# Kernel optimization log

Hardware: AMD Instinct MI355X
Metric: run time of the kernel (lower is better)

The kernel has to match this reference:

```python
import jax, jax.numpy as jnp
import numpy as np

K = 16
BN_EPS = 1e-3  # keras BatchNormalization default epsilon
LRELU_ALPHA = 0.1


def _lrelu(x):
    return jnp.where(x > 0, x, LRELU_ALPHA * x)


def _bn(x, gamma, beta):
    # training-mode batch norm over all axes except the last (channels)
    axes = tuple(range(x.ndim - 1))
    m = jnp.mean(x, axis=axes)
    v = jnp.var(x, axis=axes)
    return gamma * (x - m) * jax.lax.rsqrt(v + BN_EPS) + beta


def setup_inputs() -> dict:
    key = jax.random.key(0)
    ks = jax.random.split(key, 14)
    N, P, Cp, C0 = 32, 1024, 3, 64
    channels = [128, 128, 256]
    inp = {
        "points": jax.random.normal(ks[0], (N, P, Cp), dtype=jnp.float32),
        "features": jax.random.normal(ks[1], (N, P, C0), dtype=jnp.float32),
    }
    # edge-conv 1x1 weights (no bias, with_bn=True); glorot-ish scaling
    c_in = 2 * C0
    for i, c_out in enumerate(channels):
        scale = (2.0 / (c_in + c_out)) ** 0.5
        inp[f"W{i}"] = jax.random.normal(ks[2 + i], (c_in, c_out), dtype=jnp.float32) * scale
        inp[f"g{i}"] = jnp.ones((c_out,), dtype=jnp.float32)
        inp[f"b{i}"] = jnp.zeros((c_out,), dtype=jnp.float32)
        c_in = c_out
    # shortcut 1x1 conv C0 -> channels[-1]
    scale = (2.0 / (C0 + channels[-1])) ** 0.5
    inp["Wsc"] = jax.random.normal(ks[10], (C0, channels[-1]), dtype=jnp.float32) * scale
    inp["gsc"] = jnp.ones((channels[-1],), dtype=jnp.float32)
    inp["bsc"] = jnp.zeros((channels[-1],), dtype=jnp.float32)
    return inp


def reference(points, features, W0, g0, b0, W1, g1, b1, W2, g2, b2, Wsc, gsc, bsc):
    # pairwise squared distance matrix D: (N, P, P)
    r = jnp.sum(points * points, axis=-1)
    D = r[:, :, None] - 2.0 * jnp.einsum("npc,nqc->npq", points, points) + r[:, None, :]
    # kNN indices, excluding self (first neighbor)
    _, idx = jax.lax.top_k(-D, K + 1)
    idx = idx[:, :, 1:]  # (N, P, K)
    # gather neighbor features per batch element -> (N, P, K, C0)
    knn_fts = jax.vmap(lambda f, i: f[i])(features, idx)
    center = jnp.broadcast_to(features[:, :, None, :], knn_fts.shape)
    x = jnp.concatenate([center, knn_fts - center], axis=-1)  # (N, P, K, 2*C0)
    for W, g, b in ((W0, g0, b0), (W1, g1, b1), (W2, g2, b2)):
        x = _lrelu(_bn(jnp.einsum("npkc,cd->npkd", x, W), g, b))
    fts = jnp.mean(x, axis=2)  # average pooling over K -> (N, P, C_out)
    sc = _bn(jnp.einsum("npc,cd->npd", features, Wsc), gsc, bsc)
    return _lrelu(sc + fts)
```

## Files before the change

kernel.cpp:

```cpp
#include <hip/hip_runtime.h>
#include <stdint.h>

typedef __bf16 bf16x8 __attribute__((ext_vector_type(8)));
typedef float f32x4 __attribute__((ext_vector_type(4)));

union FragU { uint4 q; bf16x8 v; };

__device__ __forceinline__ float bf2f(uint32_t h){
  union U{uint32_t u; float f;} x; x.u = h<<16; return x.f;
}
__device__ __forceinline__ uint32_t f2bf(float f){
  union U{float f; uint32_t u;} x; x.f=f;
  return (x.u + 0x7FFFu + ((x.u>>16)&1u)) >> 16;
}
__device__ __forceinline__ float lrelu(float x){ return fmaxf(x, 0.1f*x); }

__global__ __launch_bounds__(256) void knn_kernel(const float* __restrict__ points, int* __restrict__ idx){
  __shared__ float sx[1024], sy[1024], sz[1024];
  __shared__ double srq[1024];
  __shared__ unsigned long long scand[4][64];
  const int n = blockIdx.y;
  const float* P = points + (size_t)n*1024*3;
  for(int q=threadIdx.x; q<1024; q+=256){
    float x=P[q*3+0], y=P[q*3+1], z=P[q*3+2];
    sx[q]=x; sy[q]=y; sz[q]=z;
    srq[q] = (double)x*(double)x + (double)y*(double)y + (double)z*(double)z;
  }
  __syncthreads();
  const int wv = threadIdx.x>>6;
  const int lane = threadIdx.x & 63;
  const int p = blockIdx.x*4 + wv;
  const double px=sx[p], py=sy[p], pz=sz[p];
  const double rp = srq[p];
  float key[16];
  const int prel = p - lane;
  #pragma unroll
  for(int j=0;j<16;j++){
    const int q = lane + j*64;
    double qx=sx[q], qy=sy[q], qz=sz[q];
    double dot = px*qx+py*qy+pz*qz;
    float k = fmaxf((float)((rp + srq[q]) - 2.0*dot), 0.0f);
    if(prel == j*64) k = __builtin_inff();
    key[j] = k;
  }
  float hk = key[0];
  #pragma unroll
  for(int j=1;j<16;j++) hk = fminf(hk, key[j]);
  {
    float hs = hk;
    #pragma unroll
    for(int k=2;k<=64;k<<=1){
      #pragma unroll
      for(int j=32;j>0;j>>=1){
        if(j < k){
          float o = __shfl_xor(hs, j);
          const bool keepMax = (((lane & j)!=0) ^ ((lane & k)!=0));
          hs = keepMax ? fmaxf(hs,o) : fminf(hs,o);
        }
      }
    }
    hk = hs;
  }
  const float Hk = __shfl(hk, 15);
  int cnt = 0;
  #pragma unroll
  for(int j=0;j<16;j++) cnt += (key[j] <= Hk) ? 1 : 0;
  int inc = cnt;
  #pragma unroll
  for(int d=1; d<64; d<<=1){
    int t = __shfl_up(inc, d);
    if(lane >= d) inc += t;
  }
  const int m = __shfl(inc, 63);
  const int base = inc - cnt;
  int* op = idx + ((size_t)n*1024 + p)*16;
  if(m <= 64){
    unsigned long long* sc = scand[wv];
    int slot = base;
    #pragma unroll
    for(int j=0;j<16;j++){
      if(key[j] <= Hk){
        sc[slot] = ((unsigned long long)__float_as_uint(key[j]) << 10) | (unsigned)(lane + j*64);
        slot++;
      }
    }
    unsigned long long v = (lane < m) ? sc[lane] : ~0ULL;
    #pragma unroll
    for(int k=2;k<=64;k<<=1){
      #pragma unroll
      for(int j=32;j>0;j>>=1){
        if(j < k){
          unsigned long long o = __shfl_xor(v, j);
          const bool keepMax = (((lane & j)!=0) ^ ((lane & k)!=0));
          v = keepMax ? (v > o ? v : o) : (v < o ? v : o);
        }
      }
    }
    if(lane < 16) op[lane] = (int)(v & 1023u);
  } else {
    unsigned long long e[16];
    #pragma unroll
    for(int j=0;j<16;j++)
      e[j] = ((unsigned long long)__float_as_uint(key[j]) << 10) | (unsigned)(lane + j*64);
    for(int it=0; it<16; ++it){
      unsigned long long bd = e[0];
      #pragma unroll
      for(int j=1;j<16;j++) bd = (e[j] < bd) ? e[j] : bd;
      unsigned long long pk = bd;
      #pragma unroll
      for(int s=1;s<64;s<<=1){
        unsigned long long o = __shfl_xor(pk, s);
        pk = (o < pk) ? o : pk;
      }
      #pragma unroll
      for(int j=0;j<16;j++) e[j] = (e[j]==pk) ? ~0ULL : e[j];
      if(lane==0) op[it] = (int)(pk & 1023u);
    }
  }
}

__global__ void wprep_kernel(const float* __restrict__ W0, const float* __restrict__ Wsc,
                             const float* __restrict__ W1, const float* __restrict__ W2,
                             uint16_t* __restrict__ Wpp, uint16_t* __restrict__ W1p,
                             uint16_t* __restrict__ W2p){
  const int stride = gridDim.x*blockDim.x;
  const int t0 = blockIdx.x*blockDim.x + threadIdx.x;
  for(int o=t0; o<32768; o+=stride){
    int j=o&7, l=(o>>3)&63, kc=(o>>9)&1, ct=(o>>10)&3, w=o>>12;
    int k = kc*32 + (l>>4)*8 + j;
    int c = w*64 + ct*16 + (l&15);
    float val;
    if(c<128)      val = W0[k*128+c] - W0[(k+64)*128+c];
    else if(c<256) val = W0[(k+64)*128 + (c-128)];
    else           val = Wsc[k*256 + (c-256)];
    Wpp[o] = (uint16_t)f2bf(val);
  }
  for(int o=t0; o<16384; o+=stride){
    int j=o&7, l=(o>>3)&63, kc=(o>>9)&3, ct=(o>>11)&1, w=o>>12;
    int k = kc*32 + (l>>4)*8 + j, c = w*32 + ct*16 + (l&15);
    W1p[o] = (uint16_t)f2bf(W1[k*128+c]);
  }
  for(int o=t0; o<32768; o+=stride){
    int j=o&7, l=(o>>3)&63, kc=(o>>9)&3, ct=(o>>11)&3, w=o>>13;
    int k = kc*32 + (l>>4)*8 + j, c = w*64 + ct*16 + (l&15);
    W2p[o] = (uint16_t)f2bf(W2[k*256+c]);
  }
}

__global__ __launch_bounds__(512) void proj_kernel(const float* __restrict__ feat,
    const uint16_t* __restrict__ Wpp,
    float* __restrict__ F1, float* __restrict__ F2, float* __restrict__ Fsc,
    float* __restrict__ screps){
  __shared__ alignas(16) uint16_t sA[64*64];
  const int b = blockIdx.x;
  const int tid = threadIdx.x;
  {
    const int row = tid>>3, cc = tid&7;
    const float* src = feat + ((size_t)b*64+row)*64 + cc*8;
    const float4 f0 = *(const float4*)(src);
    const float4 f1 = *(const float4*)(src+4);
    uint32_t pk[4] = { f2bf(f0.x)|(f2bf(f0.y)<<16), f2bf(f0.z)|(f2bf(f0.w)<<16),
                       f2bf(f1.x)|(f2bf(f1.y)<<16), f2bf(f1.z)|(f2bf(f1.w)<<16) };
    int bo = row*128 + cc*16; bo ^= (row&7)<<4;
    *(uint4*)((char*)sA + bo) = make_uint4(pk[0],pk[1],pk[2],pk[3]);
  }
  __syncthreads();
  const int w = tid>>6, l = tid&63;
  FragU bfr[4][2];
  #pragma unroll
  for(int ct=0;ct<4;ct++)
    #pragma unroll
    for(int kc=0;kc<2;kc++)
      bfr[ct][kc].q = *(const uint4*)(Wpp + ((size_t)((w*4+ct)*2+kc))*512 + l*8);
  f32x4 acc[4][4] = {};
  #pragma unroll
  for(int rt=0;rt<4;rt++){
    FragU a[2];
    #pragma unroll
    for(int kc=0;kc<2;kc++){
      const int row = rt*16 + (l&15);
      int bo = row*128 + kc*64 + (l>>4)*16; bo ^= (row&7)<<4;
      a[kc].q = *(const uint4*)((const char*)sA + bo);
    }
    #pragma unroll
    for(int ct=0;ct<4;ct++)
      #pragma unroll
      for(int kc=0;kc<2;kc++)
        acc[rt][ct] = __builtin_amdgcn_mfma_f32_16x16x32_bf16(a[kc].v, bfr[ct][kc].v, acc[rt][ct], 0,0,0);
  }
  #pragma unroll
  for(int rt=0;rt<4;rt++){
    #pragma unroll
    for(int ct=0;ct<4;ct++){
      const int c = w*64 + ct*16 + (l&15);
      const int rowg = b*64 + rt*16 + (l>>4)*4;
      #pragma unroll
      for(int reg=0;reg<4;reg++){
        float v = acc[rt][ct][reg];
        if(c < 128)      F1[(size_t)(rowg+reg)*128 + c] = v;
        else if(c < 256) F2[(size_t)(rowg+reg)*128 + (c-128)] = v;
        else             Fsc[(size_t)(rowg+reg)*256 + (c-256)] = v;
      }
    }
  }
  if(w>=4){
    #pragma unroll
    for(int ct=0;ct<4;ct++){
      float s=0.f, sq=0.f;
      #pragma unroll
      for(int rt=0;rt<4;rt++)
        #pragma unroll
        for(int reg=0;reg<4;reg++){ float v=acc[rt][ct][reg]; s+=v; sq+=v*v; }
      s += __shfl_xor(s,16); sq += __shfl_xor(sq,16);
      s += __shfl_xor(s,32); sq += __shfl_xor(sq,32);
      if(l<16){
        const int c = (w-4)*64 + ct*16 + l;
        atomicAdd(&screps[((b&31)*2+0)*256 + c], s);
        atomicAdd(&screps[((b&31)*2+1)*256 + c], sq);
      }
    }
  }
}

__global__ __launch_bounds__(256) void y0stats_kernel(const float* __restrict__ F1,
    const float* __restrict__ F2, const int* __restrict__ idx, float* __restrict__ reps){
  __shared__ int sIdx[256];
  const int tid = threadIdx.x;
  const int r0 = blockIdx.x*256;
  sIdx[tid] = idx[r0 + tid];
  __syncthreads();
  const int cg = tid & 31;
  const int rs = tid >> 5;
  const int nbase = (r0 >> 14) << 10;
  f32x4 s = {0,0,0,0}, sq = {0,0,0,0};
  for(int rr=0; rr<32; rr+=4){
    #pragma unroll
    for(int u=0;u<4;u++){
      const int r = rs*32 + rr + u;
      const int np = (r0 + r) >> 4;
      const int g = sIdx[r];
      const float4 a = *(const float4*)(F1 + (size_t)np*128 + cg*4);
      const float4 c = *(const float4*)(F2 + (size_t)(nbase + g)*128 + cg*4);
      float v0=a.x+c.x, v1=a.y+c.y, v2=a.z+c.z, v3=a.w+c.w;
      s[0]+=v0; s[1]+=v1; s[2]+=v2; s[3]+=v3;
      sq[0]+=v0*v0; sq[1]+=v1*v1; sq[2]+=v2*v2; sq[3]+=v3*v3;
    }
  }
  #pragma unroll
  for(int e=0;e<4;e++){
    s[e]  += __shfl_xor(s[e], 32);
    sq[e] += __shfl_xor(sq[e], 32);
  }
  if((tid&63) < 32){
    const int rep = blockIdx.x & 31;
    #pragma unroll
    for(int e=0;e<4;e++){
      atomicAdd(&reps[(rep*2+0)*128 + cg*4+e], s[e]);
      atomicAdd(&reps[(rep*2+1)*128 + cg*4+e], sq[e]);
    }
  }
}

__global__ void finalize_kernel(const float* __restrict__ reps, const float* __restrict__ gamma,
    const float* __restrict__ beta, float* __restrict__ s, float* __restrict__ t,
    int C, float inv_cnt){
  int c = threadIdx.x;
  if(c>=C) return;
  float sum=0.f, sq=0.f;
  for(int r2=0;r2<32;r2++){ sum += reps[(r2*2+0)*C + c]; sq += reps[(r2*2+1)*C + c]; }
  float m = sum*inv_cnt;
  float var = sq*inv_cnt - m*m;
  float sc = gamma[c]*rsqrtf(var + 1e-3f);
  s[c]=sc; t[c]=beta[c] - m*sc;
}

__global__ __launch_bounds__(256) void layer1_kernel(
    const float* __restrict__ F1, const float* __restrict__ F2, const int* __restrict__ idx,
    const uint16_t* __restrict__ W1p, const float* __restrict__ s0, const float* __restrict__ t0,
    uint16_t* __restrict__ y1, float* __restrict__ reps1){
  __shared__ alignas(16) uint16_t sA[64*128];
  __shared__ int sIdx[64];
  const int b = blockIdx.x;
  const int tid = threadIdx.x;
  if(tid < 64) sIdx[tid] = idx[b*64 + tid];
  const int row0 = tid>>4, q = tid&15;
  const float4 sc0a = *(const float4*)(s0 + q*8);
  const float4 sc0b = *(const float4*)(s0 + q*8 + 4);
  const float4 tt0a = *(const float4*)(t0 + q*8);
  const float4 tt0b = *(const float4*)(t0 + q*8 + 4);
  const int wv = tid>>6, l = tid&63;
  FragU bfr[2][4];
  #pragma unroll
  for(int ct=0;ct<2;ct++)
    #pragma unroll
    for(int kc=0;kc<4;kc++)
      bfr[ct][kc].q = *(const uint4*)(W1p + ((size_t)((wv*2+ct)*4+kc))*512 + l*8);
  __syncthreads();
  {
    const int npb = b*4;
    const int nbase = (b >> 8) << 10;
    int gg[4];
    #pragma unroll
    for(int jj=0;jj<4;jj++) gg[jj] = sIdx[row0 + jj*16];
    float4 va[4][4];
    #pragma unroll
    for(int jj=0;jj<4;jj++){
      const int np = npb + jj;
      const float* pf1 = F1 + (size_t)np*128 + q*8;
      const float* pf2 = F2 + (size_t)(nbase + gg[jj])*128 + q*8;
      va[jj][0] = *(const float4*)(pf1);
      va[jj][1] = *(const float4*)(pf1+4);
      va[jj][2] = *(const float4*)(pf2);
      va[jj][3] = *(const float4*)(pf2+4);
    }
    #pragma unroll
    for(int jj=0;jj<4;jj++){
      const int rw = row0 + jj*16;
      float v[8] = {va[jj][0].x+va[jj][2].x, va[jj][0].y+va[jj][2].y,
                    va[jj][0].z+va[jj][2].z, va[jj][0].w+va[jj][2].w,
                    va[jj][1].x+va[jj][3].x, va[jj][1].y+va[jj][3].y,
                    va[jj][1].z+va[jj][3].z, va[jj][1].w+va[jj][3].w};
      const float sc[8] = {sc0a.x,sc0a.y,sc0a.z,sc0a.w, sc0b.x,sc0b.y,sc0b.z,sc0b.w};
      const float tt[8] = {tt0a.x,tt0a.y,tt0a.z,tt0a.w, tt0b.x,tt0b.y,tt0b.z,tt0b.w};
      uint32_t pk[4];
      #pragma unroll
      for(int e=0;e<4;e++){
        float x0 = lrelu(sc[e*2]*v[e*2] + tt[e*2]);
        float x1 = lrelu(sc[e*2+1]*v[e*2+1] + tt[e*2+1]);
        pk[e] = f2bf(x0) | (f2bf(x1)<<16);
      }
      int bo = rw*256 + q*16; bo ^= (rw&7)<<4;
      *(uint4*)((char*)sA + bo) = make_uint4(pk[0],pk[1],pk[2],pk[3]);
    }
  }
  __syncthreads();
  f32x4 acc[4][2] = {};
  #pragma unroll
  for(int rt=0;rt<4;rt++){
    FragU a[4];
    #pragma unroll
    for(int kc=0;kc<4;kc++){
      const int rw = rt*16 + (l&15);
      int bo = rw*256 + kc*64 + (l>>4)*16; bo ^= (rw&7)<<4;
      a[kc].q = *(const uint4*)((const char*)sA + bo);
    }
    #pragma unroll
    for(int ct=0;ct<2;ct++)
      #pragma unroll
      for(int kc=0;kc<4;kc++)
        acc[rt][ct] = __builtin_amdgcn_mfma_f32_16x16x32_bf16(a[kc].v, bfr[ct][kc].v, acc[rt][ct], 0,0,0);
  }
  float ss[2]={0.f,0.f}, sq[2]={0.f,0.f};
  #pragma unroll
  for(int rt=0;rt<4;rt++)
    #pragma unroll
    for(int ct=0;ct<2;ct++)
      #pragma unroll
      for(int reg=0;reg<4;reg++){
        float v = acc[rt][ct][reg];
        ss[ct]+=v; sq[ct]+=v*v;
        const int CI = ((rt*4+wv)*2+ct)*4+reg;
        y1[(size_t)b*8192 + CI*64 + l] = (uint16_t)f2bf(v);
      }
  #pragma unroll
  for(int ct=0;ct<2;ct++){
    float a=ss[ct], b2=sq[ct];
    a += __shfl_xor(a,16); b2 += __shfl_xor(b2,16);
    a += __shfl_xor(a,32); b2 += __shfl_xor(b2,32);
    if((l>>4)==0){
      const int c = wv*32 + ct*16 + l;
      atomicAdd(&reps1[((b&31)*2+0)*128 + c], a);
      atomicAdd(&reps1[((b&31)*2+1)*128 + c], b2);
    }
  }
}

__global__ __launch_bounds__(512, 4) void layer2s_kernel(
    uint16_t* __restrict__ y1, const uint16_t* __restrict__ W2p,
    const float* __restrict__ s1, const float* __restrict__ t1,
    float* __restrict__ reps2){
  __shared__ alignas(16) uint16_t sA[2][8192];
  __shared__ float sBN[256];
  const int tid = threadIdx.x;
  const int w = tid>>6, l = tid&63;
  if(tid<128){ sBN[tid]=s1[tid]; sBN[128+tid]=t1[tid]; }
  FragU bfr[2][4];
  #pragma unroll
  for(int ct=0;ct<2;ct++)
    #pragma unroll
    for(int kc=0;kc<4;kc++)
      bfr[ct][kc].q = *(const uint4*)(W2p + ((size_t)((w*2+ct)*4+kc))*512 + l*8);
  int uc0[2], ubo[2];
  #pragma unroll
  for(int k=0;k<2;k++){
    const int u = tid + k*512;
    const int l8 = u&7, CI = u>>3;
    const int reg = CI&3, ct = (CI>>2)&1, w8 = (CI>>3)&3, rt = CI>>5;
    const int row = rt*16 + (l8>>1)*4 + reg;
    const int c0 = w8*32 + ct*16 + (l8&1)*8;
    uc0[k] = c0;
    ubo[k] = (row*256 + c0*2) ^ ((row&7)<<4);
  }
  const int bt0 = blockIdx.x*16;
  uint4 va[2];
  #pragma unroll
  for(int k=0;k<2;k++)
    va[k] = *(const uint4*)(y1 + (size_t)bt0*8192 + (size_t)(tid+k*512)*8);
  __syncthreads();
  #pragma unroll
  for(int k=0;k<2;k++){
    const float4 sa = *(const float4*)(&sBN[uc0[k]]);
    const float4 sb = *(const float4*)(&sBN[uc0[k]+4]);
    const float4 ta = *(const float4*)(&sBN[128+uc0[k]]);
    const float4 tb = *(const float4*)(&sBN[128+uc0[k]+4]);
    const float scv[8]={sa.x,sa.y,sa.z,sa.w, sb.x,sb.y,sb.z,sb.w};
    const float ttv[8]={ta.x,ta.y,ta.z,ta.w, tb.x,tb.y,tb.z,tb.w};
    const uint32_t e[4] = {va[k].x, va[k].y, va[k].z, va[k].w};
    uint32_t pk[4];
    #pragma unroll
    for(int j=0;j<4;j++){
      float x0 = lrelu(scv[j*2]*bf2f(e[j]&0xffffu) + ttv[j*2]);
      float x1 = lrelu(scv[j*2+1]*bf2f(e[j]>>16) + ttv[j*2+1]);
      pk[j] = f2bf(x0) | (f2bf(x1)<<16);
    }
    *(uint4*)((char*)sA[0] + ubo[k]) = make_uint4(pk[0],pk[1],pk[2],pk[3]);
  }
  __syncthreads();
  float ssA[2]={0,0}, sqA[2]={0,0};
  for(int t=0; t<16; ++t){
    const int bt = bt0 + t;
    const int p = t&1;
    if(t<15){
      #pragma unroll
      for(int k=0;k<2;k++)
        va[k] = *(const uint4*)(y1 + (size_t)(bt+1)*8192 + (size_t)(tid+k*512)*8);
    }
    f32x4 acc[4][2] = {};
    #pragma unroll
    for(int rt=0;rt<4;rt++){
      FragU a[4];
      #pragma unroll
      for(int kc=0;kc<4;kc++){
        const int rw = rt*16 + (l&15);
        int bo = rw*256 + kc*64 + (l>>4)*16; bo ^= (rw&7)<<4;
        a[kc].q = *(const uint4*)((const char*)sA[p] + bo);
      }
      if(w==0){
        #pragma unroll
        for(int kc=0;kc<4;kc++)
          *(uint4*)(y1 + (size_t)bt*8192 + (size_t)((rt*4+kc)*64 + l)*8) = a[kc].q;
      }
      #pragma unroll
      for(int ct=0;ct<2;ct++)
        #pragma unroll
        for(int kc=0;kc<4;kc++)
          acc[rt][ct] = __builtin_amdgcn_mfma_f32_16x16x32_bf16(a[kc].v, bfr[ct][kc].v, acc[rt][ct], 0,0,0);
    }
    #pragma unroll
    for(int ct=0;ct<2;ct++)
      #pragma unroll
      for(int rt=0;rt<4;rt++)
        #pragma unroll
        for(int reg=0;reg<4;reg++){
          float v = acc[rt][ct][reg];
          ssA[ct]+=v; sqA[ct]+=v*v;
        }
    if(t<15){
      #pragma unroll
      for(int k=0;k<2;k++){
        const float4 sa = *(const float4*)(&sBN[uc0[k]]);
        const float4 sb = *(const float4*)(&sBN[uc0[k]+4]);
        const float4 ta = *(const float4*)(&sBN[128+uc0[k]]);
        const float4 tb = *(const float4*)(&sBN[128+uc0[k]+4]);
        const float scv[8]={sa.x,sa.y,sa.z,sa.w, sb.x,sb.y,sb.z,sb.w};
        const float ttv[8]={ta.x,ta.y,ta.z,ta.w, tb.x,tb.y,tb.z,tb.w};
        const uint32_t e[4] = {va[k].x, va[k].y, va[k].z, va[k].w};
        uint32_t pk[4];
        #pragma unroll
        for(int j=0;j<4;j++){
          float x0 = lrelu(scv[j*2]*bf2f(e[j]&0xffffu) + ttv[j*2]);
          float x1 = lrelu(scv[j*2+1]*bf2f(e[j]>>16) + ttv[j*2+1]);
          pk[j] = f2bf(x0) | (f2bf(x1)<<16);
        }
        *(uint4*)((char*)sA[p^1] + ubo[k]) = make_uint4(pk[0],pk[1],pk[2],pk[3]);
      }
    }
    __syncthreads();
  }
  #pragma unroll
  for(int ct=0;ct<2;ct++){
    float a=ssA[ct], b2=sqA[ct];
    a += __shfl_xor(a,16); b2 += __shfl_xor(b2,16);
    a += __shfl_xor(a,32); b2 += __shfl_xor(b2,32);
    if((l>>4)==0){
      const int c = w*32 + ct*16 + l;
      const int rep = blockIdx.x & 31;
      atomicAdd(&reps2[(rep*2+0)*256 + c], a);
      atomicAdd(&reps2[(rep*2+1)*256 + c], b2);
    }
  }
}

__global__ __launch_bounds__(512, 4) void layer2f_kernel(
    const uint16_t* __restrict__ y1b, const uint16_t* __restrict__ W2p,
    const float* __restrict__ s2, const float* __restrict__ t2,
    const float* __restrict__ Fsc, const float* __restrict__ ssc, const float* __restrict__ tsc,
    float* __restrict__ out){
  __shared__ alignas(16) uint16_t sA[2][16384];
  const int tid = threadIdx.x;
  const int w = tid>>6, l = tid&63;
  FragU bfr[2][4];
  #pragma unroll
  for(int ct=0;ct<2;ct++)
    #pragma unroll
    for(int kc=0;kc<4;kc++)
      bfr[ct][kc].q = *(const uint4*)(W2p + ((size_t)((w*2+ct)*4+kc))*512 + l*8);
  float sc2v[2], tt2v[2], sscv[2], tscv[2];
  #pragma unroll
  for(int ct=0;ct<2;ct++){
    const int c = w*32 + ct*16 + (l&15);
    sc2v[ct]=s2[c]; tt2v[ct]=t2[c]; sscv[ct]=ssc[c]; tscv[ct]=tsc[c];
  }
  const int bt0 = blockIdx.x*16;
  {
    const uint16_t* gp = y1b + (size_t)bt0*8192 + w*512 + l*8;
    __builtin_amdgcn_global_load_lds((const uint32_t*)gp,         (uint32_t*)&sA[0][w*512 + l*8],         16, 0, 0);
    __builtin_amdgcn_global_load_lds((const uint32_t*)(gp+4096),  (uint32_t*)&sA[0][4096 + w*512 + l*8],  16, 0, 0);
    __builtin_amdgcn_global_load_lds((const uint32_t*)(gp+8192),  (uint32_t*)&sA[0][8192 + w*512 + l*8],  16, 0, 0);
    __builtin_amdgcn_global_load_lds((const uint32_t*)(gp+12288), (uint32_t*)&sA[0][12288 + w*512 + l*8], 16, 0, 0);
  }
  __syncthreads();
  for(int ph=0; ph<8; ++ph){
    const int p = ph&1;
    if(ph<7){
      const uint16_t* gp = y1b + (size_t)(bt0 + (ph+1)*2)*8192 + w*512 + l*8;
      __builtin_amdgcn_global_load_lds((const uint32_t*)gp,         (uint32_t*)&sA[p^1][w*512 + l*8],         16, 0, 0);
      __builtin_amdgcn_global_load_lds((const uint32_t*)(gp+4096),  (uint32_t*)&sA[p^1][4096 + w*512 + l*8],  16, 0, 0);
      __builtin_amdgcn_global_load_lds((const uint32_t*)(gp+8192),  (uint32_t*)&sA[p^1][8192 + w*512 + l*8],  16, 0, 0);
      __builtin_amdgcn_global_load_lds((const uint32_t*)(gp+12288), (uint32_t*)&sA[p^1][12288 + w*512 + l*8], 16, 0, 0);
    }
    #pragma unroll
    for(int tt=0; tt<2; ++tt){
      const int bt = bt0 + ph*2 + tt;
      f32x4 acc[4][2] = {};
      #pragma unroll
      for(int rt=0;rt<4;rt++){
        FragU a[4];
        #pragma unroll
        for(int kc=0;kc<4;kc++)
          a[kc].q = *(const uint4*)((const char*)sA[p] + (size_t)tt*16384 + (size_t)((rt*4+kc)*64 + l)*16);
        #pragma unroll
        for(int ct=0;ct<2;ct++)
          #pragma unroll
          for(int kc=0;kc<4;kc++)
            acc[rt][ct] = __builtin_amdgcn_mfma_f32_16x16x32_bf16(a[kc].v, bfr[ct][kc].v, acc[rt][ct], 0,0,0);
      }
      #pragma unroll
      for(int rt=0;rt<4;rt++){
        const int np = bt*4 + rt;
        #pragma unroll
        for(int ct=0;ct<2;ct++){
          const int c = w*32 + ct*16 + (l&15);
          float s=0.f;
          #pragma unroll
          for(int reg=0;reg<4;reg++) s += lrelu(sc2v[ct]*acc[rt][ct][reg] + tt2v[ct]);
          s += __shfl_xor(s,16);
          s += __shfl_xor(s,32);
          if((l>>4)==0){
            float fts = s*(1.0f/16.0f);
            float sc = sscv[ct]*Fsc[(size_t)np*256+c] + tscv[ct];
            out[(size_t)np*256+c] = lrelu(sc + fts);
          }
        }
      }
    }
    __syncthreads();
  }
}

extern "C" void kernel_launch(void* const* d_in, const int* in_sizes, int n_in,
                              void* d_out, int out_size, void* d_ws, size_t ws_size,
                              hipStream_t stream) {
  const float* points   = (const float*)d_in[0];
  const float* features = (const float*)d_in[1];
  const float* W0  = (const float*)d_in[2];
  const float* g0  = (const float*)d_in[3];
  const float* b0  = (const float*)d_in[4];
  const float* W1  = (const float*)d_in[5];
  const float* g1  = (const float*)d_in[6];
  const float* b1  = (const float*)d_in[7];
  const float* W2  = (const float*)d_in[8];
  const float* g2  = (const float*)d_in[9];
  const float* b2  = (const float*)d_in[10];
  const float* Wsc = (const float*)d_in[11];
  const float* gsc = (const float*)d_in[12];
  const float* bsc = (const float*)d_in[13];
  float* out = (float*)d_out;

  float* ws = (float*)d_ws;
  size_t off = 0;
  float* screps = ws + off; off += 16384;
  float* reps0  = ws + off; off += 8192;
  float* reps1  = ws + off; off += 8192;
  float* reps2  = ws + off; off += 16384;
  float* ssc = ws + off; off += 256;
  float* tsc = ws + off; off += 256;
  float* s0  = ws + off; off += 128;
  float* t0  = ws + off; off += 128;
  float* s1v = ws + off; off += 128;
  float* t1v = ws + off; off += 128;
  float* s2v = ws + off; off += 256;
  float* t2v = ws + off; off += 256;
  int*   idxb = (int*)(ws + off); off += 524288;
  float* F1  = ws + off; off += (size_t)32768*128;
  float* F2  = ws + off; off += (size_t)32768*128;
  float* Fsc = ws + off; off += (size_t)32768*256;
  uint16_t* W1p = (uint16_t*)(ws + off); off += 8192;
  uint16_t* W2p = (uint16_t*)(ws + off); off += 16384;
  uint16_t* Wpp = (uint16_t*)(ws + off); off += 16384;
  uint16_t* y1  = (uint16_t*)(ws + off); off += (size_t)33554432;

  hipMemsetAsync(d_ws, 0, 49152*sizeof(float), stream);

  knn_kernel<<<dim3(256,32), 256, 0, stream>>>(points, idxb);
  wprep_kernel<<<128, 256, 0, stream>>>(W0, Wsc, W1, W2, Wpp, W1p, W2p);
  proj_kernel<<<512, 512, 0, stream>>>(features, Wpp, F1, F2, Fsc, screps);
  finalize_kernel<<<1, 256, 0, stream>>>(screps, gsc, bsc, ssc, tsc, 256, 1.0f/32768.0f);
  y0stats_kernel<<<2048, 256, 0, stream>>>(F1, F2, idxb, reps0);
  finalize_kernel<<<1, 128, 0, stream>>>(reps0, g0, b0, s0, t0, 128, 1.0f/524288.0f);
  layer1_kernel<<<8192, 256, 0, stream>>>(F1, F2, idxb, W1p, s0, t0, y1, reps1);
  finalize_kernel<<<1, 128, 0, stream>>>(reps1, g1, b1, s1v, t1v, 128, 1.0f/524288.0f);
  layer2s_kernel<<<512, 512, 0, stream>>>(y1, W2p, s1v, t1v, reps2);
  finalize_kernel<<<1, 256, 0, stream>>>(reps2, g2, b2, s2v, t2v, 256, 1.0f/524288.0f);
  layer2f_kernel<<<512, 512, 0, stream>>>(y1, W2p, s2v, t2v, Fsc, ssc, tsc, out);
}
```

Before: 292.5 us.

## Make layer1 persistent with double-buffered LDS and prefetch of next tile

The layer1 kernel goes from 8192 blocks of 256 threads, each handling one 64-row tile, to 512 blocks of 512 threads that each loop over 16 tiles. The next tile's F1/F2 gather is issued before the current tile's MFMA work, and its BN/LReLU/bf16 pack is written into a second LDS buffer, so global loads overlap with matrix math. Each wave now owns 16 output channels with W1 fragments loaded once per block, and the statistics atomics are issued once per block rather than once per tile. The costs are fewer resident blocks, more registers held for prefetched data, and one block-wide barrier per tile.

```diff
diff --git a/kernel.cpp b/kernel.cpp
--- a/kernel.cpp
+++ b/kernel.cpp
@@ -274,104 +274,118 @@
   s[c]=sc; t[c]=beta[c] - m*sc;
 }
 
-__global__ __launch_bounds__(256) void layer1_kernel(
+__global__ __launch_bounds__(512) void layer1_kernel(
     const float* __restrict__ F1, const float* __restrict__ F2, const int* __restrict__ idx,
     const uint16_t* __restrict__ W1p, const float* __restrict__ s0, const float* __restrict__ t0,
     uint16_t* __restrict__ y1, float* __restrict__ reps1){
-  __shared__ alignas(16) uint16_t sA[64*128];
-  __shared__ int sIdx[64];
-  const int b = blockIdx.x;
+  __shared__ alignas(16) uint16_t sA[2][8192];
+  __shared__ int sIdx[1024];
+  const int bb = blockIdx.x;
   const int tid = threadIdx.x;
-  if(tid < 64) sIdx[tid] = idx[b*64 + tid];
-  const int row0 = tid>>4, q = tid&15;
-  const float4 sc0a = *(const float4*)(s0 + q*8);
-  const float4 sc0b = *(const float4*)(s0 + q*8 + 4);
-  const float4 tt0a = *(const float4*)(t0 + q*8);
-  const float4 tt0b = *(const float4*)(t0 + q*8 + 4);
-  const int wv = tid>>6, l = tid&63;
-  FragU bfr[2][4];
-  #pragma unroll
-  for(int ct=0;ct<2;ct++)
-    #pragma unroll
-    for(int kc=0;kc<4;kc++)
-      bfr[ct][kc].q = *(const uint4*)(W1p + ((size_t)((wv*2+ct)*4+kc))*512 + l*8);
+  const int w = tid>>6, l = tid&63;
+  sIdx[tid]      = idx[bb*1024 + tid];
+  sIdx[512+tid]  = idx[bb*1024 + 512 + tid];
+  const int row = tid>>3, q = tid&7;
+  const int nbase = (bb>>4)<<10;
+  float scv[16], ttv[16];
+  #pragma unroll
+  for(int e4=0;e4<4;e4++){
+    const float4 sv = *(const float4*)(s0 + q*16 + e4*4);
+    const float4 tv = *(const float4*)(t0 + q*16 + e4*4);
+    scv[e4*4+0]=sv.x; scv[e4*4+1]=sv.y; scv[e4*4+2]=sv.z; scv[e4*4+3]=sv.w;
+    ttv[e4*4+0]=tv.x; ttv[e4*4+1]=tv.y; ttv[e4*4+2]=tv.z; ttv[e4*4+3]=tv.w;
+  }
+  FragU bfr[4];
+  #pragma unroll
+  for(int kc=0;kc<4;kc++)
+    bfr[kc].q = *(const uint4*)(W1p + ((size_t)(w*4+kc))*512 + l*8);
   __syncthreads();
   {
-    const int npb = b*4;
-    const int nbase = (b >> 8) << 10;
-    int gg[4];
-    #pragma unroll
-    for(int jj=0;jj<4;jj++) gg[jj] = sIdx[row0 + jj*16];
-    float4 va[4][4];
-    #pragma unroll
-    for(int jj=0;jj<4;jj++){
-      const int np = npb + jj;
-      const float* pf1 = F1 + (size_t)np*128 + q*8;
-      const float* pf2 = F2 + (size_t)(nbase + gg[jj])*128 + q*8;
-      va[jj][0] = *(const float4*)(pf1);
-      va[jj][1] = *(const float4*)(pf1+4);
-      va[jj][2] = *(const float4*)(pf2);
-      va[jj][3] = *(const float4*)(pf2+4);
-    }
-    #pragma unroll
-    for(int jj=0;jj<4;jj++){
-      const int rw = row0 + jj*16;
-      float v[8] = {va[jj][0].x+va[jj][2].x, va[jj][0].y+va[jj][2].y,
-                    va[jj][0].z+va[jj][2].z, va[jj][0].w+va[jj][2].w,
-                    va[jj][1].x+va[jj][3].x, va[jj][1].y+va[jj][3].y,
-                    va[jj][1].z+va[jj][3].z, va[jj][1].w+va[jj][3].w};
-      const float sc[8] = {sc0a.x,sc0a.y,sc0a.z,sc0a.w, sc0b.x,sc0b.y,sc0b.z,sc0b.w};
-      const float tt[8] = {tt0a.x,tt0a.y,tt0a.z,tt0a.w, tt0b.x,tt0b.y,tt0b.z,tt0b.w};
-      uint32_t pk[4];
-      #pragma unroll
-      for(int e=0;e<4;e++){
-        float x0 = lrelu(sc[e*2]*v[e*2] + tt[e*2]);
-        float x1 = lrelu(sc[e*2+1]*v[e*2+1] + tt[e*2+1]);
+    const int bt = bb*16;
+    const int np = bt*4 + (row>>4);
+    const int g  = sIdx[row];
+    const float* pf1 = F1 + (size_t)np*128 + q*16;
+    const float* pf2 = F2 + (size_t)(nbase+g)*128 + q*16;
+    float4 a0=*(const float4*)(pf1), a1=*(const float4*)(pf1+4),
+           a2=*(const float4*)(pf1+8), a3=*(const float4*)(pf1+12);
+    float4 c0=*(const float4*)(pf2), c1=*(const float4*)(pf2+4),
+           c2=*(const float4*)(pf2+8), c3=*(const float4*)(pf2+12);
+    float v[16]={a0.x+c0.x,a0.y+c0.y,a0.z+c0.z,a0.w+c0.w, a1.x+c1.x,a1.y+c1.y,a1.z+c1.z,a1.w+c1.w,
+                 a2.x+c2.x,a2.y+c2.y,a2.z+c2.z,a2.w+c2.w, a3.x+c3.x,a3.y+c3.y,a3.z+c3.z,a3.w+c3.w};
+    uint32_t pk[8];
+    #pragma unroll
+    for(int e=0;e<8;e++){
+      float x0 = lrelu(scv[e*2]*v[e*2] + ttv[e*2]);
+      float x1 = lrelu(scv[e*2+1]*v[e*2+1] + ttv[e*2+1]);
+      pk[e] = f2bf(x0) | (f2bf(x1)<<16);
+    }
+    const int sw = (row&7)<<4;
+    const int bo = row*256 + q*32;
+    *(uint4*)((char*)sA[0] + (bo ^ sw))      = make_uint4(pk[0],pk[1],pk[2],pk[3]);
+    *(uint4*)((char*)sA[0] + ((bo+16) ^ sw)) = make_uint4(pk[4],pk[5],pk[6],pk[7]);
+  }
+  __syncthreads();
+  float ssA = 0.f, sqA = 0.f;
+  for(int t=0; t<16; ++t){
+    const int bt = bb*16 + t;
+    const int p = t&1;
+    float4 a0,a1,a2,a3,c0,c1,c2,c3;
+    if(t<15){
+      const int np = (bt+1)*4 + (row>>4);
+      const int g  = sIdx[(t+1)*64 + row];
+      const float* pf1 = F1 + (size_t)np*128 + q*16;
+      const float* pf2 = F2 + (size_t)(nbase+g)*128 + q*16;
+      a0=*(const float4*)(pf1); a1=*(const float4*)(pf1+4);
+      a2=*(const float4*)(pf1+8); a3=*(const float4*)(pf1+12);
+      c0=*(const float4*)(pf2); c1=*(const float4*)(pf2+4);
+      c2=*(const float4*)(pf2+8); c3=*(const float4*)(pf2+12);
+    }
+    f32x4 acc[4] = {};
+    #pragma unroll
+    for(int rt=0;rt<4;rt++){
+      FragU a[4];
+      #pragma unroll
+      for(int kc=0;kc<4;kc++){
+        const int rw = rt*16 + (l&15);
+        int bo = rw*256 + kc*64 + (l>>4)*16; bo ^= (rw&7)<<4;
+        a[kc].q = *(const uint4*)((const char*)sA[p] + bo);
+      }
+      #pragma unroll
+      for(int kc=0;kc<4;kc++)
+        acc[rt] = __builtin_amdgcn_mfma_f32_16x16x32_bf16(a[kc].v, bfr[kc].v, acc[rt], 0,0,0);
+    }
+    #pragma unroll
+    for(int rt=0;rt<4;rt++)
+      #pragma unroll
+      for(int reg=0;reg<4;reg++){
+        float v = acc[rt][reg];
+        ssA += v; sqA += v*v;
+        y1[(size_t)bt*8192 + (size_t)(((rt*8+w)*4+reg))*64 + l] = (uint16_t)f2bf(v);
+      }
+    if(t<15){
+      float v[16]={a0.x+c0.x,a0.y+c0.y,a0.z+c0.z,a0.w+c0.w, a1.x+c1.x,a1.y+c1.y,a1.z+c1.z,a1.w+c1.w,
+                   a2.x+c2.x,a2.y+c2.y,a2.z+c2.z,a2.w+c2.w, a3.x+c3.x,a3.y+c3.y,a3.z+c3.z,a3.w+c3.w};
+      uint32_t pk[8];
+      #pragma unroll
+      for(int e=0;e<8;e++){
+        float x0 = lrelu(scv[e*2]*v[e*2] + ttv[e*2]);
+        float x1 = lrelu(scv[e*2+1]*v[e*2+1] + ttv[e*2+1]);
         pk[e] = f2bf(x0) | (f2bf(x1)<<16);
       }
-      int bo = rw*256 + q*16; bo ^= (rw&7)<<4;
-      *(uint4*)((char*)sA + bo) = make_uint4(pk[0],pk[1],pk[2],pk[3]);
-    }
-  }
-  __syncthreads();
-  f32x4 acc[4][2] = {};
-  #pragma unroll
-  for(int rt=0;rt<4;rt++){
-    FragU a[4];
-    #pragma unroll
-    for(int kc=0;kc<4;kc++){
-      const int rw = rt*16 + (l&15);
-      int bo = rw*256 + kc*64 + (l>>4)*16; bo ^= (rw&7)<<4;
-      a[kc].q = *(const uint4*)((const char*)sA + bo);
-    }
-    #pragma unroll
-    for(int ct=0;ct<2;ct++)
-      #pragma unroll
-      for(int kc=0;kc<4;kc++)
-        acc[rt][ct] = __builtin_amdgcn_mfma_f32_16x16x32_bf16(a[kc].v, bfr[ct][kc].v, acc[rt][ct], 0,0,0);
-  }
-  float ss[2]={0.f,0.f}, sq[2]={0.f,0.f};
-  #pragma unroll
-  for(int rt=0;rt<4;rt++)
-    #pragma unroll
-    for(int ct=0;ct<2;ct++)
-      #pragma unroll
-      for(int reg=0;reg<4;reg++){
-        float v = acc[rt][ct][reg];
-        ss[ct]+=v; sq[ct]+=v*v;
-        const int CI = ((rt*4+wv)*2+ct)*4+reg;
-        y1[(size_t)b*8192 + CI*64 + l] = (uint16_t)f2bf(v);
-      }
-  #pragma unroll
-  for(int ct=0;ct<2;ct++){
-    float a=ss[ct], b2=sq[ct];
-    a += __shfl_xor(a,16); b2 += __shfl_xor(b2,16);
-    a += __shfl_xor(a,32); b2 += __shfl_xor(b2,32);
-    if((l>>4)==0){
-      const int c = wv*32 + ct*16 + l;
-      atomicAdd(&reps1[((b&31)*2+0)*128 + c], a);
-      atomicAdd(&reps1[((b&31)*2+1)*128 + c], b2);
-    }
+      const int sw = (row&7)<<4;
+      const int bo = row*256 + q*32;
+      *(uint4*)((char*)sA[p^1] + (bo ^ sw))      = make_uint4(pk[0],pk[1],pk[2],pk[3]);
+      *(uint4*)((char*)sA[p^1] + ((bo+16) ^ sw)) = make_uint4(pk[4],pk[5],pk[6],pk[7]);
+    }
+    __syncthreads();
+  }
+  ssA += __shfl_xor(ssA,16); sqA += __shfl_xor(sqA,16);
+  ssA += __shfl_xor(ssA,32); sqA += __shfl_xor(sqA,32);
+  if(l < 16){
+    const int c = w*16 + l;
+    const int rep = bb & 31;
+    atomicAdd(&reps1[(rep*2+0)*128 + c], ssA);
+    atomicAdd(&reps1[(rep*2+1)*128 + c], sqA);
   }
 }
 
@@ -628,7 +642,7 @@
   finalize_kernel<<<1, 256, 0, stream>>>(screps, gsc, bsc, ssc, tsc, 256, 1.0f/32768.0f);
   y0stats_kernel<<<2048, 256, 0, stream>>>(F1, F2, idxb, reps0);
   finalize_kernel<<<1, 128, 0, stream>>>(reps0, g0, b0, s0, t0, 128, 1.0f/524288.0f);
-  layer1_kernel<<<8192, 256, 0, stream>>>(F1, F2, idxb, W1p, s0, t0, y1, reps1);
+  layer1_kernel<<<512, 512, 0, stream>>>(F1, F2, idxb, W1p, s0, t0, y1, reps1);
   finalize_kernel<<<1, 128, 0, stream>>>(reps1, g1, b1, s1v, t1v, 128, 1.0f/524288.0f);
   layer2s_kernel<<<512, 512, 0, stream>>>(y1, W2p, s1v, t1v, reps2);
   finalize_kernel<<<1, 256, 0, stream>>>(reps2, g2, b2, s2v, t2v, 256, 1.0f/524288.0f);
```

Measured after the change: 300.2 us. 1.03x slower.
